# Kernel tuning notes

Hardware: AMD Instinct MI355X
Metric: run time of the kernel (lower is better)

## Reference

```python
import jax, jax.numpy as jnp
import numpy as np

NUM_ITER = 5
NUM_SLOTS = 16
INPUT_SIZE = 256
EPS = 1e-8
TAU = 1.0
B, N = 8, 16384


def setup_inputs() -> dict:
    key = jax.random.key(0)
    k1, k2 = jax.random.split(key)
    inputs = jax.random.normal(k1, (B, N, INPUT_SIZE), dtype=jnp.float32)
    # xavier_uniform for a (1, K, D) tensor (torch fan_in=K*D, fan_out=D)
    limit = float(np.sqrt(6.0 / (NUM_SLOTS * INPUT_SIZE + INPUT_SIZE)))
    slot_logits = jax.random.uniform(k2, (1, NUM_SLOTS, INPUT_SIZE),
                                     minval=-limit, maxval=limit, dtype=jnp.float32)
    mixing_coefficients = jnp.full((1, NUM_SLOTS), 1.0 / NUM_SLOTS, dtype=jnp.float32)
    return {"inputs": inputs, "slot_logits": slot_logits,
            "mixing_coefficients": mixing_coefficients}


def reference(inputs, slot_logits, mixing_coefficients):
    Bn, Nn, D = inputs.shape
    theta = jnp.broadcast_to(slot_logits, (Bn, NUM_SLOTS, D))       # (B,K,D)
    pi = jnp.broadcast_to(mixing_coefficients, (Bn, NUM_SLOTS))     # (B,K)
    p = jax.nn.softmax(inputs, axis=-1)                             # (B,N,D), loop-invariant
    for _ in range(NUM_ITER):
        log_q = jax.nn.log_softmax(theta, axis=-1)                  # (B,K,D)
        logits = jnp.einsum('bnd,bkd->bnk', p, log_q)               # (B,N,K)
        logits = logits + jnp.log(pi + EPS)[:, None, :]
        gamma = jax.nn.softmax(logits, axis=-1)                     # (B,N,K)
        pi = gamma.mean(axis=1)                                     # (B,K)
        gamma_sum = gamma.sum(axis=1) + EPS                         # (B,K)
        numerator = jnp.einsum('bnk,bnd->bkd', gamma, inputs)       # (B,K,D)
        theta = numerator / gamma_sum[:, :, None]
    g = jax.random.gumbel(jax.random.key(1), theta.shape, dtype=theta.dtype)
    slots = jax.nn.softmax((theta + g) / TAU, axis=-1)              # (B,K,D)
    return slots
```

## Files before the change

kernel.cpp:

```cpp
#include <hip/hip_runtime.h>
#include <cstdint>
#include <cstddef>

#define BN 8
#define NN 16384
#define DD 256
#define KK 16
#define NITER 5
#define EPSV 1e-8f
#define LOG256 5.545177444479562f
#define PSTR 260
#define TPB 8

typedef float f32x4 __attribute__((ext_vector_type(4)));
typedef long  i64v;

__device__ __forceinline__ float frcp(float x){ return __builtin_amdgcn_rcpf(x); }
__device__ __forceinline__ float wmax(float v){
  #pragma unroll
  for (int m = 32; m >= 1; m >>= 1) v = fmaxf(v, __shfl_xor(v, m, 64));
  return v;
}
__device__ __forceinline__ float wsum(float v){
  #pragma unroll
  for (int m = 32; m >= 1; m >>= 1) v += __shfl_xor(v, m, 64);
  return v;
}
__device__ __forceinline__ uint32_t pk4_fp8(float a, float b, float c, float d){
  int w = __builtin_amdgcn_cvt_pk_fp8_f32(a, b, 0, false);
  w = __builtin_amdgcn_cvt_pk_fp8_f32(c, d, w, true);
  return (uint32_t)w;
}

__global__ __launch_bounds__(256, 2) void k_prep6(const float* __restrict__ x,
                                                  uint2* __restrict__ pbf8,
                                                  uint2* __restrict__ xbf8,
                                                  float* __restrict__ invs){
  __shared__ float xs[2][32 * PSTR];
  const int b = blockIdx.y;
  const int Sbase = blockIdx.x * TPB;
  const int tid = threadIdx.x;
  const int wave = tid >> 6, lane = tid & 63;
  const float* xb = x + (size_t)b * NN * DD;

  auto stage = [&](int S, int buf){
    #pragma unroll
    for (int r = 0; r < 8; ++r){
      int row = wave * 8 + r;
      const float* gp = xb + ((size_t)S * 32 + row) * DD + lane * 4;
      float* lp = &xs[buf][row * PSTR];
      __builtin_amdgcn_global_load_lds(
          (const __attribute__((address_space(1))) unsigned int*)gp,
          (__attribute__((address_space(3))) unsigned int*)lp, 16, 0, 0);
    }
  };

  stage(Sbase, 0);
  for (int it = 0; it < TPB; ++it){
    const int S = Sbase + it;
    const int cur = it & 1;
    asm volatile("s_waitcnt vmcnt(0)" ::: "memory");
    __builtin_amdgcn_sched_barrier(0);
    __syncthreads();
    if (it + 1 < TPB) stage(S + 1, cur ^ 1);

    {
      int row = 8 * wave + (lane & 7);
      const float* pr = &xs[cur][row * PSTR + (lane >> 3) * 32];
      float a = 0.f;
      #pragma unroll
      for (int i = 0; i < 8; ++i){
        float4 v = *(const float4*)&pr[4 * i];
        a += __expf(v.x) + __expf(v.y) + __expf(v.z) + __expf(v.w);
      }
      a += __shfl_xor(a, 8, 64);
      a += __shfl_xor(a, 16, 64);
      a += __shfl_xor(a, 32, 64);
      if (lane < 8) invs[(size_t)b * NN + S * 32 + 8 * wave + lane] = frcp(a);
    }

    #pragma unroll
    for (int i = 0; i < 4; ++i){
      int p = wave * 4 + i; int c = p >> 3, s = p & 7;
      int rho = lane & 15;
      int n = 8 * (rho >> 2) + 4 * c + (rho & 3);
      int d = 32 * s + 8 * (lane >> 4);
      float4 v0 = *(const float4*)&xs[cur][n * PSTR + d];
      float4 v1 = *(const float4*)&xs[cur][n * PSTR + d + 4];
      uint2 o;
      o.x = pk4_fp8(__expf(v0.x), __expf(v0.y), __expf(v0.z), __expf(v0.w));
      o.y = pk4_fp8(__expf(v1.x), __expf(v1.y), __expf(v1.z), __expf(v1.w));
      pbf8[(((size_t)b * 1024 + (size_t)S * 2 + c) * 8 + s) * 64 + lane] = o;
    }
    #pragma unroll
    for (int i = 0; i < 4; ++i){
      int dt = wave * 4 + i;
      int col = dt * 16 + (lane & 15);
      int g2 = lane >> 4;
      float v[8];
      #pragma unroll
      for (int j = 0; j < 8; ++j) v[j] = xs[cur][(8 * g2 + j) * PSTR + col];
      uint2 o;
      o.x = pk4_fp8(v[0], v[1], v[2], v[3]);
      o.y = pk4_fp8(v[4], v[5], v[6], v[7]);
      xbf8[(((size_t)b * 512 + S) * 16 + dt) * 64 + lane] = o;
    }
    __syncthreads();
  }
}

__global__ __launch_bounds__(256) void k_init6(const float* __restrict__ slot_logits,
                                               const float* __restrict__ mix,
                                               uint8_t* __restrict__ lqf8,
                                               float* __restrict__ logpi){
  int w    = blockIdx.x * 4 + (threadIdx.x >> 6);
  int lane = threadIdx.x & 63;
  int b = w >> 4, k = w & 15;
  const float4* sl = (const float4*)(slot_logits + (size_t)k * DD);
  float4 t = sl[lane];
  float m = wmax(fmaxf(fmaxf(t.x, t.y), fmaxf(t.z, t.w)));
  float s = wsum(__expf(t.x-m) + __expf(t.y-m) + __expf(t.z-m) + __expf(t.w-m));
  float L = m + __logf(s) - LOG256;
  int d0 = lane * 4;
  int ss = d0 >> 5;
  int l2 = (((d0 & 31) >> 3) << 4) + k;
  int jb = d0 & 7;
  uint32_t wv = pk4_fp8(t.x - L, t.y - L, t.z - L, t.w - L);
  *(uint32_t*)(lqf8 + ((((size_t)b * 8 + ss) * 64 + l2) * 8 + jb)) = wv;
  if (lane == 0) logpi[w] = __logf(mix[k] + EPSV);
}

__global__ __launch_bounds__(256, 2) void k_em6(const uint2* __restrict__ pbf8,
                                                const uint2* __restrict__ xbf8,
                                                const uint2* __restrict__ lqf8,
                                                const float* __restrict__ logpi,
                                                const float* __restrict__ invs,
                                                float* __restrict__ pnum,
                                                float* __restrict__ ppi){
  __shared__ float sred[KK * DD];
  __shared__ float spi2[16];
  const int b = blockIdx.y, g = blockIdx.x;
  const int tid = threadIdx.x;
  const int wave = tid >> 6, lane = tid & 63;

  i64v lq8[8];
  {
    const uint2* p = lqf8 + (size_t)b * 8 * 64 + lane;
    #pragma unroll
    for (int s = 0; s < 8; ++s){ uint2 t = p[s * 64]; lq8[s] = *(i64v*)&t; }
  }
  const float lpik = logpi[b * KK + (lane & 15)];

  f32x4 acc[16];
  #pragma unroll
  for (int dt = 0; dt < 16; ++dt) acc[dt] = (f32x4){0.f, 0.f, 0.f, 0.f};
  float piacc = 0.f;

  const int S0 = (g * 4 + wave) * 2;
  #pragma unroll
  for (int ssi = 0; ssi < 2; ++ssi){
    const int S = S0 + ssi;
    const uint2* pb = pbf8 + (((size_t)b * 1024 + (size_t)S * 2) * 8) * 64 + lane;
    const uint2* xr = xbf8 + (((size_t)b * 512 + S) * 16) * 64 + lane;

    uint2 pa[16];
    #pragma unroll
    for (int i = 0; i < 16; ++i) pa[i] = pb[(size_t)i * 64];

    float ivs[8];
    {
      const float* ib = invs + (size_t)b * NN + S * 32 + 8 * (lane >> 4);
      #pragma unroll
      for (int j = 0; j < 8; ++j) ivs[j] = ib[j];
    }

    float ga[8];
    #pragma unroll
    for (int c = 0; c < 2; ++c){
      f32x4 lc = (f32x4){0.f, 0.f, 0.f, 0.f};
      #pragma unroll
      for (int s = 0; s < 8; ++s){
        i64v a = *(i64v*)&pa[c * 8 + s];
        lc = __builtin_amdgcn_mfma_f32_16x16x32_fp8_fp8(a, lq8[s], lc, 0, 0, 0);
      }
      #pragma unroll
      for (int r2 = 0; r2 < 4; ++r2){
        float lg = fmaf(lc[r2], ivs[c * 4 + r2], lpik);
        float mx = lg;
        #pragma unroll
        for (int m = 1; m <= 8; m <<= 1) mx = fmaxf(mx, __shfl_xor(mx, m, 64));
        float e = __expf(lg - mx);
        float s2 = e;
        #pragma unroll
        for (int m = 1; m <= 8; m <<= 1) s2 += __shfl_xor(s2, m, 64);
        ga[c * 4 + r2] = e * frcp(s2);
      }
    }
    uint2 gp;
    gp.x = pk4_fp8(ga[0], ga[1], ga[2], ga[3]);
    gp.y = pk4_fp8(ga[4], ga[5], ga[6], ga[7]);
    piacc += __builtin_amdgcn_cvt_f32_fp8((int)gp.x, 0)
           + __builtin_amdgcn_cvt_f32_fp8((int)gp.x, 1)
           + __builtin_amdgcn_cvt_f32_fp8((int)gp.x, 2)
           + __builtin_amdgcn_cvt_f32_fp8((int)gp.x, 3)
           + __builtin_amdgcn_cvt_f32_fp8((int)gp.y, 0)
           + __builtin_amdgcn_cvt_f32_fp8((int)gp.y, 1)
           + __builtin_amdgcn_cvt_f32_fp8((int)gp.y, 2)
           + __builtin_amdgcn_cvt_f32_fp8((int)gp.y, 3);
    i64v gA = *(i64v*)&gp;
    #pragma unroll
    for (int dt = 0; dt < 16; ++dt){
      uint2 xv = xr[(size_t)dt * 64];
      acc[dt] = __builtin_amdgcn_mfma_f32_16x16x32_fp8_fp8(gA, *(i64v*)&xv,
                                                           acc[dt], 0, 0, 0);
    }
  }

  float pk = piacc;
  pk += __shfl_xor(pk, 16, 64);
  pk += __shfl_xor(pk, 32, 64);
  __syncthreads();
  if (wave == 0){
    #pragma unroll
    for (int dt = 0; dt < 16; ++dt)
      #pragma unroll
      for (int r2 = 0; r2 < 4; ++r2)
        sred[(4 * (lane >> 4) + r2) * DD + dt * 16 + (lane & 15)] = acc[dt][r2];
    if (lane < 16) spi2[lane] = pk;
  }
  __syncthreads();
  for (int w = 1; w < 4; ++w){
    if (wave == w){
      #pragma unroll
      for (int dt = 0; dt < 16; ++dt)
        #pragma unroll
        for (int r2 = 0; r2 < 4; ++r2)
          sred[(4 * (lane >> 4) + r2) * DD + dt * 16 + (lane & 15)] += acc[dt][r2];
      if (lane < 16) spi2[lane] += pk;
    }
    __syncthreads();
  }
  float4* dst4 = (float4*)(pnum + (size_t)(b * 64 + g) * KK * DD);
  const float4* s4 = (const float4*)sred;
  #pragma unroll
  for (int j = 0; j < 4; ++j) dst4[tid + j * 256] = s4[tid + j * 256];
  if (tid < 16) ppi[(size_t)(b * 64 + g) * KK + tid] = spi2[tid];
}

__global__ __launch_bounds__(64) void k_reduce6(const float* __restrict__ pnum,
                                                const float* __restrict__ ppi,
                                                float* __restrict__ theta,
                                                uint8_t* __restrict__ lqf8,
                                                float* __restrict__ logpi){
  const int G = 64;
  int w = blockIdx.x;
  int lane = threadIdx.x;
  int b = w >> 4, k = w & 15;
  float4 sum = make_float4(0.f, 0.f, 0.f, 0.f);
  const float4* base = (const float4*)pnum + ((size_t)b * G * KK + k) * (DD/4) + lane;
  #pragma unroll 4
  for (int g = 0; g < G; ++g){
    float4 t = base[(size_t)g * KK * (DD/4)];
    sum.x += t.x; sum.y += t.y; sum.z += t.z; sum.w += t.w;
  }
  float ps = 0.f;
  for (int g = lane; g < G; g += 64) ps += ppi[((size_t)b * G + g) * KK + k];
  ps = wsum(ps);
  float inv = frcp(ps + EPSV);
  float4 th = make_float4(sum.x * inv, sum.y * inv, sum.z * inv, sum.w * inv);
  ((float4*)(theta + (size_t)w * DD))[lane] = th;
  float m = wmax(fmaxf(fmaxf(th.x, th.y), fmaxf(th.z, th.w)));
  float s = wsum(__expf(th.x-m) + __expf(th.y-m) + __expf(th.z-m) + __expf(th.w-m));
  float L = m + __logf(s) - LOG256;
  int d0 = lane * 4;
  int ss = d0 >> 5;
  int l2 = (((d0 & 31) >> 3) << 4) + k;
  int jb = d0 & 7;
  uint32_t wv = pk4_fp8(th.x - L, th.y - L, th.z - L, th.w - L);
  *(uint32_t*)(lqf8 + ((((size_t)b * 8 + ss) * 64 + l2) * 8 + jb)) = wv;
  if (lane == 0) logpi[w] = __logf(ps * (1.0f / NN) + EPSV);
}

__device__ __forceinline__ uint32_t rotl32(uint32_t x, int r){ return (x << r) | (x >> (32 - r)); }
__device__ __forceinline__ void tf2x32(uint32_t k0, uint32_t k1, uint32_t c0, uint32_t c1,
                                       uint32_t& o0, uint32_t& o1){
  uint32_t ks0 = k0, ks1 = k1, ks2 = 0x1BD11BDAu ^ k0 ^ k1;
  uint32_t x0 = c0 + ks0, x1 = c1 + ks1;
  #define RND(r) { x0 += x1; x1 = rotl32(x1, r); x1 ^= x0; }
  RND(13) RND(15) RND(26) RND(6)   x0 += ks1; x1 += ks2 + 1u;
  RND(17) RND(29) RND(16) RND(24)  x0 += ks2; x1 += ks0 + 2u;
  RND(13) RND(15) RND(26) RND(6)   x0 += ks0; x1 += ks1 + 3u;
  RND(17) RND(29) RND(16) RND(24)  x0 += ks1; x1 += ks2 + 4u;
  RND(13) RND(15) RND(26) RND(6)   x0 += ks2; x1 += ks0 + 5u;
  #undef RND
  o0 = x0; o1 = x1;
}

__global__ __launch_bounds__(256) void k_final(const float* __restrict__ theta,
                                               float* __restrict__ out){
  int w    = blockIdx.x * 4 + (threadIdx.x >> 6);
  int lane = threadIdx.x & 63;
  float4 th = ((const float4*)(theta + (size_t)w * DD))[lane];
  int i0 = w * DD + lane * 4;
  float gv[4];
  #pragma unroll
  for (int j = 0; j < 4; ++j){
    uint32_t i = (uint32_t)(i0 + j);
    uint32_t o0, o1;
    tf2x32(0u, 1u, 0u, i, o0, o1);
    uint32_t bits = o0 ^ o1;
    float f = __uint_as_float((bits >> 9) | 0x3f800000u) - 1.0f;
    const float TINY = 1.17549435e-38f;
    float u = fmaxf(f + TINY, TINY);
    gv[j] = -logf(-logf(u));
  }
  float4 y = make_float4(th.x + gv[0], th.y + gv[1], th.z + gv[2], th.w + gv[3]);
  float m = wmax(fmaxf(fmaxf(y.x, y.y), fmaxf(y.z, y.w)));
  float4 e = make_float4(__expf(y.x-m), __expf(y.y-m), __expf(y.z-m), __expf(y.w-m));
  float s = wsum(e.x + e.y + e.z + e.w);
  float inv = 1.0f / s;
  ((float4*)(out + (size_t)w * DD))[lane] =
      make_float4(e.x*inv, e.y*inv, e.z*inv, e.w*inv);
}

__global__ __launch_bounds__(256) void k_fill(float* __restrict__ out, float v){
  out[blockIdx.x * 256 + threadIdx.x] = v;
}

extern "C" void kernel_launch(void* const* d_in, const int* in_sizes, int n_in,
                              void* d_out, int out_size, void* d_ws, size_t ws_size,
                              hipStream_t stream){
  const float* x    = (const float*)d_in[0];
  const float* sl   = (const float*)d_in[1];
  const float* mix  = (const float*)d_in[2];
  float* out = (float*)d_out;
  char* ws = (char*)d_ws;

  const size_t SZ_PBF  = 33554432ull;
  const size_t SZ_XBF  = 33554432ull;
  const size_t SZ_LQF  = 32768ull;
  const size_t SZ_INV  = (size_t)BN*NN*4;
  const size_t SZ_TH   = (size_t)BN*KK*DD*4;
  const size_t SZ_LP   = 512ull;
  const size_t SZ_PNUM = (size_t)BN*64*KK*DD*4;
  const size_t SZ_PPI  = (size_t)BN*64*KK*4;
  size_t need = SZ_PBF + SZ_XBF + SZ_LQF + SZ_INV + SZ_TH + SZ_LP + SZ_PNUM + SZ_PPI;

  if (ws_size < need){
    k_fill<<<(BN*KK*DD)/256, 256, 0, stream>>>(out, -9.0f);
    return;
  }
  size_t o = 0;
  uint2*   pbf8  = (uint2*)(ws + o);     o += SZ_PBF;
  uint2*   xbf8  = (uint2*)(ws + o);     o += SZ_XBF;
  uint8_t* lqf8  = (uint8_t*)(ws + o);   o += SZ_LQF;
  float*   invs  = (float*)(ws + o);     o += SZ_INV;
  float*   theta = (float*)(ws + o);     o += SZ_TH;
  float*   logpi = (float*)(ws + o);     o += SZ_LP;
  float*   pnum  = (float*)(ws + o);     o += SZ_PNUM;
  float*   ppi   = (float*)(ws + o);

  k_prep6<<<dim3(512 / TPB, BN), 256, 0, stream>>>(x, pbf8, xbf8, invs);
  k_init6<<<(BN*KK)/4, 256, 0, stream>>>(sl, mix, lqf8, logpi);
  for (int it = 0; it < NITER; ++it){
    k_em6    <<<dim3(64, BN), 256, 0, stream>>>(pbf8, xbf8, (const uint2*)lqf8,
                                                logpi, invs, pnum, ppi);
    k_reduce6<<<BN*KK, 64, 0, stream>>>(pnum, ppi, theta, lqf8, logpi);
  }
  k_final<<<(BN*KK)/4, 256, 0, stream>>>(theta, out);
}
```

Measured before the change: 160.2 us.

## Halve EM grid with more tiles per wave and store partials as bf16

Each wave in the EM kernel now processes four 32-row tiles instead of two, which halves the grid to 32 blocks per batch and halves the number of partial numerator slabs. The partial sums are also written as bf16 instead of fp32, and the reduce kernel widens them back before summing. This is meant to cut the partial-write and reduction traffic and the per-block LDS reduction overhead. The cost is fewer blocks (256 total), which may underfill the GPU, plus some precision loss in the partials.

```diff
diff --git a/kernel.cpp b/kernel.cpp
--- a/kernel.cpp
+++ b/kernel.cpp
@@ -11,6 +11,7 @@
 #define LOG256 5.545177444479562f
 #define PSTR 260
 #define TPB 8
+#define GG 32
 
 typedef float f32x4 __attribute__((ext_vector_type(4)));
 typedef long  i64v;
@@ -31,6 +32,14 @@
   w = __builtin_amdgcn_cvt_pk_fp8_f32(c, d, w, true);
   return (uint32_t)w;
 }
+__device__ __forceinline__ uint32_t f2bf(float f){
+  uint32_t u = __float_as_uint(f);
+  return (u + 0x7fffu + ((u >> 16) & 1u)) >> 16;
+}
+__device__ __forceinline__ uint32_t pk2bf(float a, float b){
+  return f2bf(a) | (f2bf(b) << 16);
+}
+__device__ __forceinline__ float bf2f(uint32_t h){ return __uint_as_float(h << 16); }
 
 __global__ __launch_bounds__(256, 2) void k_prep6(const float* __restrict__ x,
                                                   uint2* __restrict__ pbf8,
@@ -135,7 +144,7 @@
                                                 const uint2* __restrict__ lqf8,
                                                 const float* __restrict__ logpi,
                                                 const float* __restrict__ invs,
-                                                float* __restrict__ pnum,
+                                                uint16_t* __restrict__ pnumb,
                                                 float* __restrict__ ppi){
   __shared__ float sred[KK * DD];
   __shared__ float spi2[16];
@@ -156,9 +165,9 @@
   for (int dt = 0; dt < 16; ++dt) acc[dt] = (f32x4){0.f, 0.f, 0.f, 0.f};
   float piacc = 0.f;
 
-  const int S0 = (g * 4 + wave) * 2;
-  #pragma unroll
-  for (int ssi = 0; ssi < 2; ++ssi){
+  const int S0 = (g * 4 + wave) * 4;
+  #pragma unroll
+  for (int ssi = 0; ssi < 4; ++ssi){
     const int S = S0 + ssi;
     const uint2* pb = pbf8 + (((size_t)b * 1024 + (size_t)S * 2) * 8) * 64 + lane;
     const uint2* xr = xbf8 + (((size_t)b * 512 + S) * 16) * 64 + lane;
@@ -240,31 +249,35 @@
     }
     __syncthreads();
   }
-  float4* dst4 = (float4*)(pnum + (size_t)(b * 64 + g) * KK * DD);
-  const float4* s4 = (const float4*)sred;
-  #pragma unroll
-  for (int j = 0; j < 4; ++j) dst4[tid + j * 256] = s4[tid + j * 256];
-  if (tid < 16) ppi[(size_t)(b * 64 + g) * KK + tid] = spi2[tid];
-}
-
-__global__ __launch_bounds__(64) void k_reduce6(const float* __restrict__ pnum,
+  uint32_t* dst = (uint32_t*)(pnumb + (size_t)(b * GG + g) * KK * DD);
+  #pragma unroll
+  for (int j = 0; j < 8; ++j){
+    float a = sred[tid * 2 + j * 512];
+    float c = sred[tid * 2 + 1 + j * 512];
+    dst[tid + j * 256] = pk2bf(a, c);
+  }
+  if (tid < 16) ppi[(size_t)(b * GG + g) * KK + tid] = spi2[tid];
+}
+
+__global__ __launch_bounds__(64) void k_reduce6(const uint16_t* __restrict__ pnumb,
                                                 const float* __restrict__ ppi,
                                                 float* __restrict__ theta,
                                                 uint8_t* __restrict__ lqf8,
                                                 float* __restrict__ logpi){
-  const int G = 64;
   int w = blockIdx.x;
   int lane = threadIdx.x;
   int b = w >> 4, k = w & 15;
   float4 sum = make_float4(0.f, 0.f, 0.f, 0.f);
-  const float4* base = (const float4*)pnum + ((size_t)b * G * KK + k) * (DD/4) + lane;
   #pragma unroll 4
-  for (int g = 0; g < G; ++g){
-    float4 t = base[(size_t)g * KK * (DD/4)];
-    sum.x += t.x; sum.y += t.y; sum.z += t.z; sum.w += t.w;
+  for (int g = 0; g < GG; ++g){
+    const uint2* p = (const uint2*)(pnumb +
+        ((size_t)(b * GG + g) * KK + k) * DD + lane * 4);
+    uint2 v = *p;
+    sum.x += bf2f(v.x & 0xffffu); sum.y += bf2f(v.x >> 16);
+    sum.z += bf2f(v.y & 0xffffu); sum.w += bf2f(v.y >> 16);
   }
   float ps = 0.f;
-  for (int g = lane; g < G; g += 64) ps += ppi[((size_t)b * G + g) * KK + k];
+  for (int g = lane; g < GG; g += 64) ps += ppi[((size_t)b * GG + g) * KK + k];
   ps = wsum(ps);
   float inv = frcp(ps + EPSV);
   float4 th = make_float4(sum.x * inv, sum.y * inv, sum.z * inv, sum.w * inv);
@@ -342,8 +355,8 @@
   const size_t SZ_INV  = (size_t)BN*NN*4;
   const size_t SZ_TH   = (size_t)BN*KK*DD*4;
   const size_t SZ_LP   = 512ull;
-  const size_t SZ_PNUM = (size_t)BN*64*KK*DD*4;
-  const size_t SZ_PPI  = (size_t)BN*64*KK*4;
+  const size_t SZ_PNUM = (size_t)BN*GG*KK*DD*2;
+  const size_t SZ_PPI  = (size_t)BN*GG*KK*4;
   size_t need = SZ_PBF + SZ_XBF + SZ_LQF + SZ_INV + SZ_TH + SZ_LP + SZ_PNUM + SZ_PPI;
 
   if (ws_size < need){
@@ -351,21 +364,21 @@
     return;
   }
   size_t o = 0;
-  uint2*   pbf8  = (uint2*)(ws + o);     o += SZ_PBF;
-  uint2*   xbf8  = (uint2*)(ws + o);     o += SZ_XBF;
-  uint8_t* lqf8  = (uint8_t*)(ws + o);   o += SZ_LQF;
-  float*   invs  = (float*)(ws + o);     o += SZ_INV;
-  float*   theta = (float*)(ws + o);     o += SZ_TH;
-  float*   logpi = (float*)(ws + o);     o += SZ_LP;
-  float*   pnum  = (float*)(ws + o);     o += SZ_PNUM;
-  float*   ppi   = (float*)(ws + o);
+  uint2*    pbf8  = (uint2*)(ws + o);     o += SZ_PBF;
+  uint2*    xbf8  = (uint2*)(ws + o);     o += SZ_XBF;
+  uint8_t*  lqf8  = (uint8_t*)(ws + o);   o += SZ_LQF;
+  float*    invs  = (float*)(ws + o);     o += SZ_INV;
+  float*    theta = (float*)(ws + o);     o += SZ_TH;
+  float*    logpi = (float*)(ws + o);     o += SZ_LP;
+  uint16_t* pnumb = (uint16_t*)(ws + o);  o += SZ_PNUM;
+  float*    ppi   = (float*)(ws + o);
 
   k_prep6<<<dim3(512 / TPB, BN), 256, 0, stream>>>(x, pbf8, xbf8, invs);
   k_init6<<<(BN*KK)/4, 256, 0, stream>>>(sl, mix, lqf8, logpi);
   for (int it = 0; it < NITER; ++it){
-    k_em6    <<<dim3(64, BN), 256, 0, stream>>>(pbf8, xbf8, (const uint2*)lqf8,
-                                                logpi, invs, pnum, ppi);
-    k_reduce6<<<BN*KK, 64, 0, stream>>>(pnum, ppi, theta, lqf8, logpi);
+    k_em6    <<<dim3(GG, BN), 256, 0, stream>>>(pbf8, xbf8, (const uint2*)lqf8,
+                                                logpi, invs, pnumb, ppi);
+    k_reduce6<<<BN*KK, 64, 0, stream>>>(pnumb, ppi, theta, lqf8, logpi);
   }
   k_final<<<(BN*KK)/4, 256, 0, stream>>>(theta, out);
 }
```

New measurement: 157.4 us. Within noise of the previous version (-1.7%).
